# Kernel tuning notes

Measured on AMD Instinct MI355X. Metric: run time of the kernel, lower is better.

## Reference

```python
import jax, jax.numpy as jnp
from jax import lax
import numpy as np

B, N, C = 4, 2000, 80           # images, proposals/img, foreground classes
SCORE_THR = 0.05
IOU_THR = 0.5
MAX_PER_IMG = 100
K_PRE = 2000                     # pre-NMS top-k candidates per image
STDS = np.array([0.1, 0.1, 0.2, 0.2], dtype=np.float32)
MAX_RATIO = float(abs(np.log(16.0 / 1000.0)))  # wh_ratio_clip=16/1000


def setup_inputs() -> dict:
    key = jax.random.key(0)
    k1, k2, k3 = jax.random.split(key, 3)
    class_outs = jax.random.normal(k1, (B, N, C + 1), dtype=jnp.float32)
    regression_outs = jax.random.normal(k2, (B, N, C * 4), dtype=jnp.float32) * 0.5
    # random valid proposal boxes inside 800x1333 images (x1<x2, y1<y2)
    xy = jax.random.uniform(k3, (B, N, 2, 2), dtype=jnp.float32)
    xy = xy * jnp.array([1333.0, 800.0], dtype=jnp.float32)
    lo = jnp.min(xy, axis=2)
    hi = jnp.max(xy, axis=2) + 1.0
    boxes = jnp.concatenate([lo, hi], axis=-1)  # [B,N,4] x1,y1,x2,y2
    images_hw = jnp.tile(jnp.array([[800, 1333]], dtype=jnp.int32), (B, 1))
    return {"class_outs": class_outs, "regression_outs": regression_outs,
            "boxes": boxes, "images_hw": images_hw}


def _decode(props, deltas, h, w):
    # props [N,4], deltas [N,C,4] -> decoded boxes [N,C,4], clipped to image
    d = deltas * jnp.asarray(STDS)
    dx, dy, dw, dh = d[..., 0], d[..., 1], d[..., 2], d[..., 3]
    dw = jnp.clip(dw, -MAX_RATIO, MAX_RATIO)
    dh = jnp.clip(dh, -MAX_RATIO, MAX_RATIO)
    px = (props[:, None, 0] + props[:, None, 2]) * 0.5
    py = (props[:, None, 1] + props[:, None, 3]) * 0.5
    pw = props[:, None, 2] - props[:, None, 0]
    ph = props[:, None, 3] - props[:, None, 1]
    gx = px + pw * dx
    gy = py + ph * dy
    gw = pw * jnp.exp(dw)
    gh = ph * jnp.exp(dh)
    x1 = jnp.clip(gx - gw * 0.5, 0.0, w)
    y1 = jnp.clip(gy - gh * 0.5, 0.0, h)
    x2 = jnp.clip(gx + gw * 0.5, 0.0, w)
    y2 = jnp.clip(gy + gh * 0.5, 0.0, h)
    return jnp.stack([x1, y1, x2, y2], axis=-1)


def _pairwise_iou(b):
    # b [K,4] -> iou [K,K]
    area = (b[:, 2] - b[:, 0]) * (b[:, 3] - b[:, 1])
    lt = jnp.maximum(b[:, None, :2], b[None, :, :2])
    rb = jnp.minimum(b[:, None, 2:], b[None, :, 2:])
    wh = jnp.clip(rb - lt, 0.0)
    inter = wh[..., 0] * wh[..., 1]
    return inter / (area[:, None] + area[None, :] - inter + 1e-6)


def _process_image(cls_out, reg_out, props, hw):
    h = hw[0].astype(jnp.float32)
    w = hw[1].astype(jnp.float32)
    scores = jax.nn.softmax(cls_out, axis=-1)[:, :C]          # drop background col
    bboxes = _decode(props, reg_out.reshape(N, C, 4), h, w)   # [N,C,4]
    flat_scores = scores.reshape(-1)                          # [N*C]
    flat_boxes = bboxes.reshape(-1, 4)
    labels = jnp.tile(jnp.arange(C, dtype=jnp.int32), N)      # class fastest-varying
    cand = jnp.where(flat_scores > SCORE_THR, flat_scores, -1.0)
    top_scores, top_idx = lax.top_k(cand, K_PRE)
    top_boxes = flat_boxes[top_idx]
    top_labels = labels[top_idx]
    valid = top_scores > SCORE_THR
    # class-offset trick: boxes of distinct classes never overlap
    off = top_labels.astype(jnp.float32)[:, None] * (jnp.maximum(h, w) + 1.0)
    iou = _pairwise_iou(top_boxes + off)                      # [K_PRE,K_PRE]
    idxs = jnp.arange(K_PRE)

    def body(i, keep):
        sup = (idxs > i) & (iou[i] > IOU_THR) & keep[i]
        return keep & ~sup

    keep = lax.fori_loop(0, K_PRE, body, valid)
    kept_scores = jnp.where(keep, top_scores, -1.0)
    det_scores, det_i = lax.top_k(kept_scores, MAX_PER_IMG)
    det_valid = det_scores > SCORE_THR
    det_boxes = jnp.where(det_valid[:, None], top_boxes[det_i], 0.0)
    det_labels = jnp.where(det_valid, top_labels[det_i], -1)
    det_scores = jnp.where(det_valid, det_scores, 0.0)
    return det_boxes, det_scores, det_labels


def reference(class_outs, regression_outs, boxes, images_hw):
    det_boxes, det_scores, det_labels = jax.vmap(_process_image)(
        class_outs, regression_outs, boxes, images_hw)
    return det_boxes, det_scores, det_labels
```

## Files before the change

### kernel.cpp

```cpp
#include <hip/hip_runtime.h>


typedef unsigned long long u64;
typedef unsigned int u32;

#define B_ 4
#define N_ 2000
#define C_ 80
#define NCLS 81
#define KPRE 2000
#define MAXDET 100
#define TARGET 192
#define NB 2312
#define NBPAD 2368
#define NG 37
#define HBASE 0xF500
#define KSHIFT 46
#define CAPA 256
#define CAPB 2048
#define CAPIMG 8192
#define KPT 8
#define BPI 125
#define BIGI 0x7fffffff

#define WS_GCUR  0
#define WS_GHIST 64
#define WS_GFLAG 37952
#define WS_GKEYS 38016
#define WS_ZEND  37952

__device__ __forceinline__ u64 pack_key(float score, unsigned fi) {
  return ((u64)__float_as_uint(score) << 32) | (u64)(0xFFFFFFFFu - fi);
}
__device__ __forceinline__ int bucket_of_bits(u32 sb) {
  return min(max((int)(sb >> 14) - HBASE, 0), NB - 1);
}

__device__ __forceinline__ float wred_max(float v) {
  int t;
#define STEPM(ctrl)                                                          \
  t = __builtin_amdgcn_update_dpp(__float_as_int(v), __float_as_int(v),      \
                                  (ctrl), 0xF, 0xF, false);                  \
  v = fmaxf(v, __int_as_float(t));
  STEPM(0x111) STEPM(0x112) STEPM(0x114) STEPM(0x118) STEPM(0x142) STEPM(0x143)
#undef STEPM
  return __int_as_float(__builtin_amdgcn_readlane(__float_as_int(v), 63));
}
__device__ __forceinline__ float wred_sum(float v) {
  int t;
#define STEPS(ctrl)                                                          \
  t = __builtin_amdgcn_update_dpp(0, __float_as_int(v), (ctrl), 0xF, 0xF,    \
                                  false);                                    \
  v = v + __int_as_float(t);
  STEPS(0x111) STEPS(0x112) STEPS(0x114) STEPS(0x118) STEPS(0x142) STEPS(0x143)
#undef STEPS
  return __int_as_float(__builtin_amdgcn_readlane(__float_as_int(v), 63));
}

__device__ __forceinline__ int dpp_min8(int v) {
  int t;
  t = __builtin_amdgcn_update_dpp(BIGI, v, 0x104, 0xF, 0xF, false);
  v = min(v, t);
  t = __builtin_amdgcn_update_dpp(BIGI, v, 0x102, 0xF, 0xF, false);
  v = min(v, t);
  t = __builtin_amdgcn_update_dpp(BIGI, v, 0x101, 0xF, 0xF, false);
  v = min(v, t);
  return v;
}

__device__ __forceinline__ float4 decode_one(
    u64 kk, const float* __restrict__ reg, const float* __restrict__ props,
    int b, float h, float w, float offscale) {
  const float MAXR = 4.135166556742356f;
  unsigned fi = 0xFFFFFFFFu - (u32)kk;
  int n = (int)(fi / (unsigned)C_);
  int c = (int)(fi - (unsigned)n * (unsigned)C_);
  float4 p = ((const float4*)props)[b * N_ + n];
  const float* dl = reg + ((size_t)(b * N_ + n)) * (C_ * 4) + c * 4;
  float dx = dl[0] * 0.1f;
  float dy = dl[1] * 0.1f;
  float dw = fminf(fmaxf(dl[2] * 0.2f, -MAXR), MAXR);
  float dh = fminf(fmaxf(dl[3] * 0.2f, -MAXR), MAXR);
  float px = (p.x + p.z) * 0.5f, py = (p.y + p.w) * 0.5f;
  float pw = p.z - p.x, ph = p.w - p.y;
  float gx = px + pw * dx, gy = py + ph * dy;
  float gw = pw * expf(dw), gh = ph * expf(dh);
  float off = (float)c * offscale;
  return make_float4(fminf(fmaxf(gx - gw * 0.5f, 0.0f), w) + off,
                     fminf(fmaxf(gy - gh * 0.5f, 0.0f), h) + off,
                     fminf(fmaxf(gx + gw * 0.5f, 0.0f), w) + off,
                     fminf(fmaxf(gy + gh * 0.5f, 0.0f), h) + off);
}

__global__ __launch_bounds__(1024) void cand_kernel(
    const float* __restrict__ cls, u64* __restrict__ gkeys,
    u32* __restrict__ gcur, u32* __restrict__ ghist) {
  __shared__ int s_wc[16], s_woff[16];
  __shared__ int s_base;
  const int tid = threadIdx.x;
  const int w = tid >> 6, lane = tid & 63;
  const int blk = blockIdx.x;
  const int b = blk / BPI;
  const int n = (blk % BPI) * 16 + w;
  const float* lg = cls + (size_t)(b * N_ + n) * NCLS;
  float x0 = lg[lane];
  float x1 = (lane < 17) ? lg[64 + lane] : -3.0e38f;
  float mx = wred_max(fmaxf(x0, x1));
  float e0 = expf(x0 - mx);
  float e1 = (lane < 17) ? expf(x1 - mx) : 0.0f;
  float sum = wred_sum(e0 + e1);
  float sc0 = e0 / sum, sc1 = e1 / sum;
  bool p0 = sc0 > 0.05f;
  bool p1 = (lane < 16) && (sc1 > 0.05f);
  u64 m0 = __ballot(p0), m1 = __ballot(p1);
  int c0 = __popcll(m0);
  if (lane == 0) s_wc[w] = c0 + __popcll(m1);
  __syncthreads();
  if (tid == 0) {
    int acc = 0;
#pragma unroll
    for (int i = 0; i < 16; ++i) { s_woff[i] = acc; acc += s_wc[i]; }
    s_base = (acc > 0) ? (int)atomicAdd(&gcur[b], (u32)acc) : 0;
  }
  __syncthreads();
  const int base = s_base + s_woff[w];
  const u64 lt = (1ull << lane) - 1;
  u64* gk = gkeys + (size_t)b * CAPIMG;
  u32* gh = ghist + (size_t)b * NBPAD;
  if (p0) {
    int slot = base + __popcll(m0 & lt);
    if (slot < CAPIMG) gk[slot] = pack_key(sc0, (unsigned)(n * C_ + lane));
    atomicAdd(&gh[bucket_of_bits(__float_as_uint(sc0))], 1u);
  }
  if (p1) {
    int slot = base + c0 + __popcll(m1 & lt);
    if (slot < CAPIMG) gk[slot] = pack_key(sc1, (unsigned)(n * C_ + 64 + lane));
    atomicAdd(&gh[bucket_of_bits(__float_as_uint(sc1))], 1u);
  }
}

__global__ __launch_bounds__(1024) void nmsA_kernel(
    const float* __restrict__ reg, const float* __restrict__ props,
    const int* __restrict__ hw, const u64* __restrict__ gkeys,
    const u32* __restrict__ gcur, const u32* __restrict__ ghist,
    int* __restrict__ gflag, float* __restrict__ out) {
  __shared__ u64 lds8[2156];
  char* bp = (char*)lds8;
  u64* SS = (u64*)bp;
  u64* U = (u64*)(bp + 2048);
  u64* rb = (u64*)(bp + 4128);
  float4* bxA = (float4*)(bp + 12320);
  int* outl = (int*)(bp + 16416);
  int* misc = (int*)(bp + 16928);
  int* s_coarse = (int*)(bp + 16992);

  const int b = blockIdx.x, tid = threadIdx.x;
  const int wv = tid >> 6, lane = tid & 63;

  float h = (float)hw[b * 2 + 0];
  float w = (float)hw[b * 2 + 1];
  float offscale = fmaxf(h, w) + 1.0f;

  if (tid < 16) misc[tid] = 0;
  if (tid >= NG && tid < 64) s_coarse[tid] = 0;

  const u64* keys = gkeys + (size_t)b * CAPIMG;
  const u32 Mraw = gcur[b];
  const int M = min((int)Mraw, CAPIMG);
  if (tid == 0 && Mraw > (u32)CAPIMG) misc[7] = 1;
  u64 kreg[KPT];
#pragma unroll
  for (int r = 0; r < KPT; r++) {
    int idx = tid + (r << 10);
    kreg[r] = (idx < M) ? keys[idx] : 0ULL;
  }
  if (wv >= 12) {
    int g0 = (wv == 12) ? 0 : 10 + (wv - 13) * 9;
    int g1 = (wv == 12) ? 10 : g0 + 9;
    for (int g2 = g0; g2 < g1; g2++) {
      int v = (int)ghist[b * NBPAD + ((g2 << 6) | lane)];
#pragma unroll
      for (int o = 32; o; o >>= 1) v += __shfl_xor(v, o);
      if (lane == 0) s_coarse[g2] = v;
    }
  }
  __syncthreads();

  if (tid < 64) {
    int v = s_coarse[lane];
#pragma unroll
    for (int off = 1; off < 64; off <<= 1) {
      int src = lane + off;
      int o = __shfl(v, src < 64 ? src : 63);
      if (src < 64) v += o;
    }
    int Mtot = __shfl(v, 0);
    u64 pm = __ballot(v >= TARGET);
    int T_A = 0, S_A;
    if (pm) {
      int gs = 63 - __builtin_clzll(pm);
      int beyond = __shfl(v, gs + 1);
      int fv = (int)ghist[b * NBPAD + ((gs << 6) | lane)];
#pragma unroll
      for (int off = 1; off < 64; off <<= 1) {
        int src = lane + off;
        int o = __shfl(fv, src < 64 ? src : 63);
        if (src < 64) fv += o;
      }
      int cum = beyond + fv;
      u64 pm2 = __ballot(cum >= TARGET);
      int tr = 63 - __builtin_clzll(pm2);
      T_A = (gs << 6) + tr;
      S_A = __shfl(cum, tr);
    } else {
      S_A = Mtot;
    }
    if (lane == 0) { misc[0] = T_A; misc[2] = S_A; misc[3] = Mtot; }
  }
  __syncthreads();

  const int T_A = misc[0], S_A = misc[2], Mtot = misc[3];
  bool modeB = (S_A > CAPA) || (misc[7] != 0);
  int K = 0, nkept = 0;

  if (!modeB) {
    {
      const u64 lt = (1ull << lane) - 1;
#pragma unroll
      for (int r = 0; r < KPT; r++) {
        int idx = tid + (r << 10);
        bool pr = (idx < M) &&
                  (bucket_of_bits((u32)(kreg[r] >> 32)) >= T_A);
        u64 mk = __ballot(pr);
        if (mk) {
          int wbase = 0;
          if (lane == 0) wbase = atomicAdd(&misc[4], __popcll(mk));
          wbase = __shfl(wbase, 0);
          if (pr) {
            int pos = wbase + __popcll(mk & lt);
            if (pos < CAPA) U[pos] = kreg[r];
          }
        }
      }
    }
    __syncthreads();
    int S = misc[4];
    if (S > CAPA) S = CAPA;

    if (tid == 0 && (S & 1)) U[S] = 0ULL;
    __syncthreads();
    if (tid < S) {
      u64 k1 = U[tid];
      int r1 = 0;
      const ulonglong2* Uu2 = (const ulonglong2*)U;
      int half = (S + 1) >> 1;
      for (int k = 0; k < half; k++) {
        ulonglong2 kk = Uu2[k];
        r1 += (kk.x > k1) + (kk.y > k1);
      }
      SS[r1] = k1;
    }
    __syncthreads();
    K = S;
    for (int j = tid; j < K; j += 1024)
      bxA[j] = decode_one(SS[j], reg, props, b, h, w, offscale);
    __syncthreads();

    int nwords = (S + 63) >> 6;
    int ntiles = nwords * (nwords + 1) / 2;
    for (int t = wv; t < ntiles; t += 16) {
      int ti = 0, rem = t;
      while (rem >= nwords - ti) { rem -= nwords - ti; ti++; }
      int tj = ti + rem;
      int i = (ti << 6) + lane;
      float4 bi4 = bxA[i];
      float ai = (bi4.z - bi4.x) * (bi4.w - bi4.y);
      u64 bits = 0;
      int jbase = tj << 6;
      int jcount = min(64, S - jbase);
      for (int jj = 0; jj < jcount; jj++) {
        int j = jbase + jj;
        float4 bj = bxA[j];
        float aj = (bj.z - bj.x) * (bj.w - bj.y);
        float iw = fmaxf(fminf(bi4.z, bj.z) - fmaxf(bi4.x, bj.x), 0.0f);
        float ih = fmaxf(fminf(bi4.w, bj.w) - fmaxf(bi4.y, bj.y), 0.0f);
        float inter = iw * ih;
        float iou = inter / (ai + aj - inter + 1e-6f);
        if (j > i && iou > 0.5f) bits |= (1ull << jj);
      }
      if (i < S) rb[i * 4 + tj] = bits;
    }
    __syncthreads();

    if (tid < 64) {
      int nw7 = (S + 63) >> 6;
      u64 alive = 0;
      if (lane < nw7) {
        alive = ~0ull;
        int remb = S & 63;
        if (lane == nw7 - 1 && remb) alive = (1ull << remb) - 1;
      }
      int nk = 0;
      if (S > 0) {
        int i = 0;
        u64 row = (lane < nw7) ? rb[0 * 4 + lane] : 0ull;
        for (;;) {
          if (lane == 0) outl[nk] = i;
          nk++;
          if (nk >= MAXDET) break;
          if (lane == (i >> 6)) alive &= ~(1ull << (i & 63));
          u64 rowSpec = (i + 1 < S && lane < nw7) ? rb[(i + 1) * 4 + lane] : 0ull;
          u64 a2 = alive & ~row;
          alive = a2;
          int cnd = a2 ? ((lane << 6) + (int)__builtin_ctzll(a2)) : BIGI;
          int m8 = dpp_min8(cnd);
          int ni = __builtin_amdgcn_readfirstlane(m8);
          if (ni >= BIGI) break;
          row = (ni == i + 1) ? rowSpec
                              : ((lane < nw7) ? rb[ni * 4 + lane] : 0ull);
          i = ni;
        }
      }
      if (lane == 0) misc[6] = nk;
    }
    __syncthreads();
    nkept = misc[6];
    if (nkept < MAXDET && K < Mtot && K < KPRE) modeB = true;
  }

  if (tid == 0) gflag[b] = modeB ? 1 : 0;
  if (modeB) return;

  float* oBox = out;
  float* oSc = out + B_ * MAXDET * 4;
  float* oLb = out + B_ * MAXDET * 5;
  for (int k2 = tid; k2 < MAXDET; k2 += 1024) {
    float4 bb = make_float4(0.0f, 0.0f, 0.0f, 0.0f);
    float sv = 0.0f, lv = -1.0f;
    if (k2 < nkept) {
      int idx = outl[k2];
      u64 kk = SS[idx];
      sv = __uint_as_float((u32)(kk >> 32));
      unsigned fi = 0xFFFFFFFFu - (u32)kk;
      int c = (int)(fi % (unsigned)C_);
      float off = (float)c * offscale;
      float4 ob = bxA[idx];
      bb = make_float4(ob.x - off, ob.y - off, ob.z - off, ob.w - off);
      lv = (float)c;
    }
    oBox[(b * MAXDET + k2) * 4 + 0] = bb.x;
    oBox[(b * MAXDET + k2) * 4 + 1] = bb.y;
    oBox[(b * MAXDET + k2) * 4 + 2] = bb.z;
    oBox[(b * MAXDET + k2) * 4 + 3] = bb.w;
    oSc[b * MAXDET + k2] = sv;
    oLb[b * MAXDET + k2] = lv;
  }
}

__global__ __launch_bounds__(1024) void nmsB_kernel(
    const float* __restrict__ reg, const float* __restrict__ props,
    const int* __restrict__ hw, const u64* __restrict__ gkeys,
    const u32* __restrict__ gcur, const int* __restrict__ gflag,
    float* __restrict__ out) {
  const int b = blockIdx.x, tid = threadIdx.x;
  if (gflag[b] == 0) return;

  __shared__ u64 lds8[7952];
  char* bp = (char*)lds8;
  u32* hist = (u32*)(bp + 0);
  u64* U2 = (u64*)(bp + 9472);
  u64* SSB = (u64*)(bp + 25856);
  int* outl = (int*)(bp + 42240);
  int* misc = (int*)(bp + 42752);
  const int lane = tid & 63;

  float h = (float)hw[b * 2 + 0];
  float w = (float)hw[b * 2 + 1];
  float offscale = fmaxf(h, w) + 1.0f;

  const u64* keys = gkeys + (size_t)b * CAPIMG;
  const int M = min((int)gcur[b], CAPIMG);

  for (int i = tid; i < NBPAD; i += 1024) hist[i] = 0;
  if (tid < 16) misc[tid] = 0;
  __syncthreads();

  for (int idx = tid; idx < M; idx += 1024) {
    u64 key = keys[idx];
    int bi = min(max((int)(key >> KSHIFT) - HBASE, 0), NB - 1);
    atomicAdd(&hist[bi], 1u);
  }
  __syncthreads();

  if (tid == 0) {
    int acc = 0, tb = 0;
    for (int bi = NB - 1; bi >= 0; bi--) {
      acc += (int)hist[bi];
      if (acc >= KPRE) { tb = bi; break; }
    }
    if (acc > CAPB) tb = min(tb + 1, NB - 1);
    misc[1] = tb;
    misc[4] = 0;
  }
  __syncthreads();
  int T_B = misc[1];

  for (int idx0 = 0; idx0 < M; idx0 += 1024) {
    int idx = idx0 + tid;
    bool pred = false;
    u64 key = 0;
    if (idx < M) {
      key = keys[idx];
      int bi = min(max((int)(key >> KSHIFT) - HBASE, 0), NB - 1);
      pred = (bi >= T_B);
    }
    u64 mk = __ballot(pred);
    if (mk) {
      int wbase = 0;
      if (lane == 0) wbase = atomicAdd(&misc[4], __popcll(mk));
      wbase = __shfl(wbase, 0);
      if (pred) {
        int pos = wbase + __popcll(mk & ((1ull << lane) - 1));
        if (pos < CAPB) U2[pos] = key;
      }
    }
  }
  __syncthreads();
  int S = misc[4];
  if (S > CAPB) S = CAPB;
  {
    int j1 = tid, j2 = tid + 1024;
    u64 k1 = (j1 < S) ? U2[j1] : 0ULL;
    u64 k2 = (j2 < S) ? U2[j2] : 0ULL;
    int r1 = 0, r2 = 0;
    for (int k = 0; k < S; k++) {
      u64 kk = U2[k];
      r1 += (kk > k1);
      r2 += (kk > k2);
    }
    __syncthreads();
    if (j1 < S) SSB[r1] = k1;
    if (j2 < S) SSB[r2] = k2;
  }
  __syncthreads();
  int K = (S < KPRE) ? S : KPRE;
  int j1 = tid, j2 = tid + 1024;
  bool kp1 = (j1 < K), kp2 = (j2 < K);
  float4 bb1 = kp1 ? decode_one(SSB[j1], reg, props, b, h, w, offscale)
                   : make_float4(0, 0, 0, 0);
  float4 bb2 = kp2 ? decode_one(SSB[j2], reg, props, b, h, w, offscale)
                   : make_float4(0, 0, 0, 0);
  int nk = 0;
  if (K > 0) {
    int i = 0;
    for (;;) {
      if (tid == 0) { outl[nk] = i; misc[5] = K; }
      nk++;
      if (nk >= MAXDET) break;
      __syncthreads();
      float4 tb = decode_one(SSB[i], reg, props, b, h, w, offscale);
      float ai = (tb.z - tb.x) * (tb.w - tb.y);
      int ln = K;
      if (kp1 && j1 > i) {
        float aj = (bb1.z - bb1.x) * (bb1.w - bb1.y);
        float iw = fmaxf(fminf(tb.z, bb1.z) - fmaxf(tb.x, bb1.x), 0.0f);
        float ih = fmaxf(fminf(tb.w, bb1.w) - fmaxf(tb.y, bb1.y), 0.0f);
        float inter = iw * ih;
        float iou = inter / (ai + aj - inter + 1e-6f);
        if (iou > 0.5f) kp1 = false;
        else ln = min(ln, j1);
      }
      if (kp2 && j2 > i) {
        float aj = (bb2.z - bb2.x) * (bb2.w - bb2.y);
        float iw = fmaxf(fminf(tb.z, bb2.z) - fmaxf(tb.x, bb2.x), 0.0f);
        float ih = fmaxf(fminf(tb.w, bb2.w) - fmaxf(tb.y, bb2.y), 0.0f);
        float inter = iw * ih;
        float iou = inter / (ai + aj - inter + 1e-6f);
        if (iou > 0.5f) kp2 = false;
        else ln = min(ln, j2);
      }
#pragma unroll
      for (int off = 32; off; off >>= 1) ln = min(ln, __shfl_xor(ln, off));
      if ((tid & 63) == 0 && ln < K) atomicMin(&misc[5], ln);
      __syncthreads();
      int ni = misc[5];
      __syncthreads();
      if (ni >= K) break;
      i = ni;
    }
  }
  if (tid == 0) misc[6] = nk;
  __syncthreads();
  int nkept = misc[6];

  float* oBox = out;
  float* oSc = out + B_ * MAXDET * 4;
  float* oLb = out + B_ * MAXDET * 5;
  for (int k2 = tid; k2 < MAXDET; k2 += 1024) {
    float4 bb = make_float4(0.0f, 0.0f, 0.0f, 0.0f);
    float sv = 0.0f, lv = -1.0f;
    if (k2 < nkept) {
      int idx = outl[k2];
      u64 kk = SSB[idx];
      sv = __uint_as_float((u32)(kk >> 32));
      unsigned fi = 0xFFFFFFFFu - (u32)kk;
      int c = (int)(fi % (unsigned)C_);
      float off = (float)c * offscale;
      float4 ob = decode_one(kk, reg, props, b, h, w, offscale);
      bb = make_float4(ob.x - off, ob.y - off, ob.z - off, ob.w - off);
      lv = (float)c;
    }
    oBox[(b * MAXDET + k2) * 4 + 0] = bb.x;
    oBox[(b * MAXDET + k2) * 4 + 1] = bb.y;
    oBox[(b * MAXDET + k2) * 4 + 2] = bb.z;
    oBox[(b * MAXDET + k2) * 4 + 3] = bb.w;
    oSc[b * MAXDET + k2] = sv;
    oLb[b * MAXDET + k2] = lv;
  }
}

extern "C" void kernel_launch(void* const* d_in, const int* in_sizes, int n_in,
                              void* d_out, int out_size, void* d_ws, size_t ws_size,
                              hipStream_t stream) {
  const float* cls = (const float*)d_in[0];
  const float* reg = (const float*)d_in[1];
  const float* props = (const float*)d_in[2];
  const int* hw = (const int*)d_in[3];
  float* out = (float*)d_out;

  u32* gcur = (u32*)((char*)d_ws + WS_GCUR);
  u32* ghist = (u32*)((char*)d_ws + WS_GHIST);
  int* gflag = (int*)((char*)d_ws + WS_GFLAG);
  u64* gkeys = (u64*)((char*)d_ws + WS_GKEYS);

  hipMemsetAsync(d_ws, 0, WS_ZEND, stream);
  cand_kernel<<<B_ * BPI, 1024, 0, stream>>>(cls, gkeys, gcur, ghist);
  nmsA_kernel<<<B_, 1024, 0, stream>>>(reg, props, hw, gkeys, gcur, ghist,
                                       gflag, out);
  nmsB_kernel<<<B_, 1024, 0, stream>>>(reg, props, hw, gkeys, gcur, gflag, out);
}
```

Measured before the change: 109.5 us.

## Split NMS fast path into mask-build and scan kernels; overlap decode with rank sort

Splits the fast-path NMS into two kernels. The first builds the suppression bitmask and writes sorted keys, boxes and mask rows to workspace. A new 256-thread kernel then runs the serial greedy scan and writes the outputs. Box decoding now runs on unsorted candidates in parallel with the rank sort and is scattered into sorted order afterwards. The histogram is cached in LDS, and key loads no longer wait on the candidate count. This adds a kernel launch and a global round trip for the intermediates, so the gain relies on the shorter per-kernel critical path.

Result: no change. 110.4 us (+0.9%).

```diff
diff --git a/kernel.cpp b/kernel.cpp
--- a/kernel.cpp
+++ b/kernel.cpp
@@ -26,7 +26,11 @@
 #define WS_GCUR  0
 #define WS_GHIST 64
 #define WS_GFLAG 37952
-#define WS_GKEYS 38016
+#define WS_GMETA 37968
+#define WS_GSS   38016
+#define WS_GBX   46208
+#define WS_GRB   62592
+#define WS_GKEYS 95360
 #define WS_ZEND  37952
 
 __device__ __forceinline__ u64 pack_key(float score, unsigned fi) {
@@ -143,16 +147,19 @@
     const float* __restrict__ reg, const float* __restrict__ props,
     const int* __restrict__ hw, const u64* __restrict__ gkeys,
     const u32* __restrict__ gcur, const u32* __restrict__ ghist,
-    int* __restrict__ gflag, float* __restrict__ out) {
-  __shared__ u64 lds8[2156];
+    int* __restrict__ gflag, int* __restrict__ gmeta,
+    u64* __restrict__ gss, float4* __restrict__ gbx, u64* __restrict__ grb) {
+  __shared__ u64 lds8[3914];
   char* bp = (char*)lds8;
-  u64* SS = (u64*)bp;
-  u64* U = (u64*)(bp + 2048);
-  u64* rb = (u64*)(bp + 4128);
-  float4* bxA = (float4*)(bp + 12320);
-  int* outl = (int*)(bp + 16416);
-  int* misc = (int*)(bp + 16928);
-  int* s_coarse = (int*)(bp + 16992);
+  u64* U = (u64*)bp;
+  u64* SS = (u64*)(bp + 2064);
+  u64* rb = (u64*)(bp + 4112);
+  float4* bxU = (float4*)(bp + 12304);
+  float4* bxA = (float4*)(bp + 16400);
+  u32* s_hist = (u32*)(bp + 20496);
+  int* rankA = (int*)(bp + 29968);
+  int* s_coarse = (int*)(bp + 30992);
+  int* misc = (int*)(bp + 31248);
 
   const int b = blockIdx.x, tid = threadIdx.x;
   const int wv = tid >> 6, lane = tid & 63;
@@ -165,20 +172,20 @@
   if (tid >= NG && tid < 64) s_coarse[tid] = 0;
 
   const u64* keys = gkeys + (size_t)b * CAPIMG;
-  const u32 Mraw = gcur[b];
-  const int M = min((int)Mraw, CAPIMG);
-  if (tid == 0 && Mraw > (u32)CAPIMG) misc[7] = 1;
   u64 kreg[KPT];
 #pragma unroll
-  for (int r = 0; r < KPT; r++) {
-    int idx = tid + (r << 10);
-    kreg[r] = (idx < M) ? keys[idx] : 0ULL;
+  for (int r = 0; r < KPT; r++) kreg[r] = keys[tid + (r << 10)];
+  if (tid == 0) {
+    u32 Mraw = gcur[b];
+    misc[5] = min((int)Mraw, CAPIMG);
+    if (Mraw > (u32)CAPIMG) misc[7] = 1;
   }
   if (wv >= 12) {
     int g0 = (wv == 12) ? 0 : 10 + (wv - 13) * 9;
     int g1 = (wv == 12) ? 10 : g0 + 9;
     for (int g2 = g0; g2 < g1; g2++) {
       int v = (int)ghist[b * NBPAD + ((g2 << 6) | lane)];
+      s_hist[(g2 << 6) | lane] = (u32)v;
 #pragma unroll
       for (int o = 32; o; o >>= 1) v += __shfl_xor(v, o);
       if (lane == 0) s_coarse[g2] = v;
@@ -200,7 +207,7 @@
     if (pm) {
       int gs = 63 - __builtin_clzll(pm);
       int beyond = __shfl(v, gs + 1);
-      int fv = (int)ghist[b * NBPAD + ((gs << 6) | lane)];
+      int fv = (int)s_hist[(gs << 6) | lane];
 #pragma unroll
       for (int off = 1; off < 64; off <<= 1) {
         int src = lane + off;
@@ -219,36 +226,37 @@
   }
   __syncthreads();
 
-  const int T_A = misc[0], S_A = misc[2], Mtot = misc[3];
-  bool modeB = (S_A > CAPA) || (misc[7] != 0);
-  int K = 0, nkept = 0;
-
-  if (!modeB) {
-    {
-      const u64 lt = (1ull << lane) - 1;
-#pragma unroll
-      for (int r = 0; r < KPT; r++) {
-        int idx = tid + (r << 10);
-        bool pr = (idx < M) &&
-                  (bucket_of_bits((u32)(kreg[r] >> 32)) >= T_A);
-        u64 mk = __ballot(pr);
-        if (mk) {
-          int wbase = 0;
-          if (lane == 0) wbase = atomicAdd(&misc[4], __popcll(mk));
-          wbase = __shfl(wbase, 0);
-          if (pr) {
-            int pos = wbase + __popcll(mk & lt);
-            if (pos < CAPA) U[pos] = kreg[r];
-          }
+  const int T_A = misc[0], S_A = misc[2], Mtot = misc[3], M = misc[5];
+  if (S_A > CAPA || misc[7] != 0) {
+    if (tid == 0) gflag[b] = 1;
+    return;
+  }
+
+  {
+    const u64 lt = (1ull << lane) - 1;
+#pragma unroll
+    for (int r = 0; r < KPT; r++) {
+      int idx = tid + (r << 10);
+      bool pr = (idx < M) && (bucket_of_bits((u32)(kreg[r] >> 32)) >= T_A);
+      u64 mk = __ballot(pr);
+      if (mk) {
+        int wbase = 0;
+        if (lane == 0) wbase = atomicAdd(&misc[4], __popcll(mk));
+        wbase = __shfl(wbase, 0);
+        if (pr) {
+          int pos = wbase + __popcll(mk & lt);
+          if (pos < CAPA) U[pos] = kreg[r];
         }
       }
     }
-    __syncthreads();
-    int S = misc[4];
-    if (S > CAPA) S = CAPA;
-
-    if (tid == 0 && (S & 1)) U[S] = 0ULL;
-    __syncthreads();
+  }
+  __syncthreads();
+  int S = misc[4];
+  if (S > CAPA) S = CAPA;
+  if (tid == 0 && (S & 1)) U[S] = 0ULL;
+  __syncthreads();
+
+  if (tid < 256) {
     if (tid < S) {
       u64 k1 = U[tid];
       int r1 = 0;
@@ -258,93 +266,139 @@
         ulonglong2 kk = Uu2[k];
         r1 += (kk.x > k1) + (kk.y > k1);
       }
+      rankA[tid] = r1;
       SS[r1] = k1;
     }
-    __syncthreads();
-    K = S;
-    for (int j = tid; j < K; j += 1024)
-      bxA[j] = decode_one(SS[j], reg, props, b, h, w, offscale);
-    __syncthreads();
-
-    int nwords = (S + 63) >> 6;
-    int ntiles = nwords * (nwords + 1) / 2;
-    for (int t = wv; t < ntiles; t += 16) {
-      int ti = 0, rem = t;
-      while (rem >= nwords - ti) { rem -= nwords - ti; ti++; }
-      int tj = ti + rem;
-      int i = (ti << 6) + lane;
-      float4 bi4 = bxA[i];
-      float ai = (bi4.z - bi4.x) * (bi4.w - bi4.y);
-      u64 bits = 0;
-      int jbase = tj << 6;
-      int jcount = min(64, S - jbase);
-      for (int jj = 0; jj < jcount; jj++) {
-        int j = jbase + jj;
-        float4 bj = bxA[j];
-        float aj = (bj.z - bj.x) * (bj.w - bj.y);
-        float iw = fmaxf(fminf(bi4.z, bj.z) - fmaxf(bi4.x, bj.x), 0.0f);
-        float ih = fmaxf(fminf(bi4.w, bj.w) - fmaxf(bi4.y, bj.y), 0.0f);
-        float inter = iw * ih;
-        float iou = inter / (ai + aj - inter + 1e-6f);
-        if (j > i && iou > 0.5f) bits |= (1ull << jj);
+  } else if (tid < 512) {
+    int j = tid - 256;
+    if (j < S) bxU[j] = decode_one(U[j], reg, props, b, h, w, offscale);
+  }
+  __syncthreads();
+  if (tid < S) bxA[rankA[tid]] = bxU[tid];
+  __syncthreads();
+
+  int nwords = (S + 63) >> 6;
+  int ntiles = nwords * (nwords + 1) / 2;
+  for (int t = wv; t < ntiles; t += 16) {
+    int ti = 0, rem = t;
+    while (rem >= nwords - ti) { rem -= nwords - ti; ti++; }
+    int tj = ti + rem;
+    int i = (ti << 6) + lane;
+    float4 bi4 = bxA[i];
+    float ai = (bi4.z - bi4.x) * (bi4.w - bi4.y);
+    u64 bits = 0;
+    int jbase = tj << 6;
+    int jcount = min(64, S - jbase);
+    for (int jj = 0; jj < jcount; jj++) {
+      int j = jbase + jj;
+      float4 bj = bxA[j];
+      float aj = (bj.z - bj.x) * (bj.w - bj.y);
+      float iw = fmaxf(fminf(bi4.z, bj.z) - fmaxf(bi4.x, bj.x), 0.0f);
+      float ih = fmaxf(fminf(bi4.w, bj.w) - fmaxf(bi4.y, bj.y), 0.0f);
+      float inter = iw * ih;
+      float iou = inter / (ai + aj - inter + 1e-6f);
+      if (j > i && iou > 0.5f) bits |= (1ull << jj);
+    }
+    if (i < S) rb[i * 4 + tj] = bits;
+  }
+  __syncthreads();
+
+  if (tid < 256) {
+    if (tid < S) gss[b * CAPA + tid] = SS[tid];
+  } else if (tid < 512) {
+    int j = tid - 256;
+    if (j < S) gbx[b * CAPA + j] = bxA[j];
+  }
+  {
+    int i = tid >> 2, wd = tid & 3;
+    if (i < S) grb[b * CAPA * 4 + i * 4 + wd] = rb[i * 4 + wd];
+  }
+  if (tid == 0) {
+    gmeta[b * 2 + 0] = S;
+    gmeta[b * 2 + 1] = Mtot;
+    gflag[b] = 0;
+  }
+}
+
+__global__ __launch_bounds__(256) void scan_kernel(
+    const int* __restrict__ hw, int* __restrict__ gflag,
+    const int* __restrict__ gmeta, const u64* __restrict__ gss,
+    const float4* __restrict__ gbx, const u64* __restrict__ grb,
+    float* __restrict__ out) {
+  __shared__ u64 lds8[1096];
+  char* bp = (char*)lds8;
+  u64* rb = (u64*)bp;
+  int* outl = (int*)(bp + 8192);
+  int* s_nk = (int*)(bp + 8704);
+
+  const int b = blockIdx.x, tid = threadIdx.x;
+  const int lane = tid & 63;
+  if (gflag[b] != 0) return;
+
+  const int S = gmeta[b * 2 + 0];
+  const int Mtot = gmeta[b * 2 + 1];
+#pragma unroll
+  for (int r = 0; r < 4; r++) {
+    int idx = tid + (r << 8);
+    rb[idx] = grb[b * CAPA * 4 + idx];
+  }
+  float h = (float)hw[b * 2 + 0];
+  float w = (float)hw[b * 2 + 1];
+  float offscale = fmaxf(h, w) + 1.0f;
+  __syncthreads();
+
+  if (tid < 64) {
+    int nw7 = (S + 63) >> 6;
+    u64 alive = 0;
+    if (lane < nw7) {
+      alive = ~0ull;
+      int remb = S & 63;
+      if (lane == nw7 - 1 && remb) alive = (1ull << remb) - 1;
+    }
+    int nk = 0;
+    if (S > 0) {
+      int i = 0;
+      u64 row = (lane < nw7) ? rb[0 * 4 + lane] : 0ull;
+      for (;;) {
+        if (lane == 0) outl[nk] = i;
+        nk++;
+        if (nk >= MAXDET) break;
+        if (lane == (i >> 6)) alive &= ~(1ull << (i & 63));
+        u64 rowSpec = (i + 1 < S && lane < nw7) ? rb[(i + 1) * 4 + lane] : 0ull;
+        u64 a2 = alive & ~row;
+        alive = a2;
+        int cnd = a2 ? ((lane << 6) + (int)__builtin_ctzll(a2)) : BIGI;
+        int m8 = dpp_min8(cnd);
+        int ni = __builtin_amdgcn_readfirstlane(m8);
+        if (ni >= BIGI) break;
+        row = (ni == i + 1) ? rowSpec
+                            : ((lane < nw7) ? rb[ni * 4 + lane] : 0ull);
+        i = ni;
       }
-      if (i < S) rb[i * 4 + tj] = bits;
-    }
-    __syncthreads();
-
-    if (tid < 64) {
-      int nw7 = (S + 63) >> 6;
-      u64 alive = 0;
-      if (lane < nw7) {
-        alive = ~0ull;
-        int remb = S & 63;
-        if (lane == nw7 - 1 && remb) alive = (1ull << remb) - 1;
-      }
-      int nk = 0;
-      if (S > 0) {
-        int i = 0;
-        u64 row = (lane < nw7) ? rb[0 * 4 + lane] : 0ull;
-        for (;;) {
-          if (lane == 0) outl[nk] = i;
-          nk++;
-          if (nk >= MAXDET) break;
-          if (lane == (i >> 6)) alive &= ~(1ull << (i & 63));
-          u64 rowSpec = (i + 1 < S && lane < nw7) ? rb[(i + 1) * 4 + lane] : 0ull;
-          u64 a2 = alive & ~row;
-          alive = a2;
-          int cnd = a2 ? ((lane << 6) + (int)__builtin_ctzll(a2)) : BIGI;
-          int m8 = dpp_min8(cnd);
-          int ni = __builtin_amdgcn_readfirstlane(m8);
-          if (ni >= BIGI) break;
-          row = (ni == i + 1) ? rowSpec
-                              : ((lane < nw7) ? rb[ni * 4 + lane] : 0ull);
-          i = ni;
-        }
-      }
-      if (lane == 0) misc[6] = nk;
-    }
-    __syncthreads();
-    nkept = misc[6];
-    if (nkept < MAXDET && K < Mtot && K < KPRE) modeB = true;
-  }
-
-  if (tid == 0) gflag[b] = modeB ? 1 : 0;
-  if (modeB) return;
+    }
+    if (lane == 0) *s_nk = nk;
+  }
+  __syncthreads();
+  const int nkept = *s_nk;
+  if (nkept < MAXDET && S < Mtot && S < KPRE) {
+    if (tid == 0) gflag[b] = 1;
+    return;
+  }
 
   float* oBox = out;
   float* oSc = out + B_ * MAXDET * 4;
   float* oLb = out + B_ * MAXDET * 5;
-  for (int k2 = tid; k2 < MAXDET; k2 += 1024) {
+  for (int k2 = tid; k2 < MAXDET; k2 += 256) {
     float4 bb = make_float4(0.0f, 0.0f, 0.0f, 0.0f);
     float sv = 0.0f, lv = -1.0f;
     if (k2 < nkept) {
       int idx = outl[k2];
-      u64 kk = SS[idx];
+      u64 kk = gss[b * CAPA + idx];
       sv = __uint_as_float((u32)(kk >> 32));
       unsigned fi = 0xFFFFFFFFu - (u32)kk;
       int c = (int)(fi % (unsigned)C_);
       float off = (float)c * offscale;
-      float4 ob = bxA[idx];
+      float4 ob = gbx[b * CAPA + idx];
       bb = make_float4(ob.x - off, ob.y - off, ob.z - off, ob.w - off);
       lv = (float)c;
     }
@@ -531,11 +585,16 @@
   u32* gcur = (u32*)((char*)d_ws + WS_GCUR);
   u32* ghist = (u32*)((char*)d_ws + WS_GHIST);
   int* gflag = (int*)((char*)d_ws + WS_GFLAG);
+  int* gmeta = (int*)((char*)d_ws + WS_GMETA);
+  u64* gss = (u64*)((char*)d_ws + WS_GSS);
+  float4* gbx = (float4*)((char*)d_ws + WS_GBX);
+  u64* grb = (u64*)((char*)d_ws + WS_GRB);
   u64* gkeys = (u64*)((char*)d_ws + WS_GKEYS);
 
   hipMemsetAsync(d_ws, 0, WS_ZEND, stream);
   cand_kernel<<<B_ * BPI, 1024, 0, stream>>>(cls, gkeys, gcur, ghist);
   nmsA_kernel<<<B_, 1024, 0, stream>>>(reg, props, hw, gkeys, gcur, ghist,
-                                       gflag, out);
+                                       gflag, gmeta, gss, gbx, grb);
+  scan_kernel<<<B_, 256, 0, stream>>>(hw, gflag, gmeta, gss, gbx, grb, out);
   nmsB_kernel<<<B_, 1024, 0, stream>>>(reg, props, hw, gkeys, gcur, gflag, out);
 }
```

## Decode candidate boxes in candidate kernel and stream keys in NMS kernel

Applied to the files above, without the earlier changes.

Box decoding moves from the single-block-per-image NMS kernel into the massively parallel candidate kernel. Each candidate's decoded, class-offset box is written to a new workspace buffer, and the NMS kernel gathers the boxes by slot index after ranking. The NMS kernel also caches the histogram in LDS instead of re-reading global memory, and streams keys with one-ahead prefetch instead of holding eight in registers. This takes the dependent reg/props gathers and exp math off the serial critical path. The cost is extra global writes for every candidate passing the threshold, not just the top few hundred.

Result: no change. 109.6 us (+0.1%).

```diff
diff --git a/kernel.cpp b/kernel.cpp
--- a/kernel.cpp
+++ b/kernel.cpp
@@ -22,11 +22,13 @@
 #define KPT 8
 #define BPI 125
 #define BIGI 0x7fffffff
+#define MAXR 4.135166556742356f
 
 #define WS_GCUR  0
 #define WS_GHIST 64
 #define WS_GFLAG 37952
 #define WS_GKEYS 38016
+#define WS_GBOX  300160
 #define WS_ZEND  37952
 
 __device__ __forceinline__ u64 pack_key(float score, unsigned fi) {
@@ -71,7 +73,6 @@
 __device__ __forceinline__ float4 decode_one(
     u64 kk, const float* __restrict__ reg, const float* __restrict__ props,
     int b, float h, float w, float offscale) {
-  const float MAXR = 4.135166556742356f;
   unsigned fi = 0xFFFFFFFFu - (u32)kk;
   int n = (int)(fi / (unsigned)C_);
   int c = (int)(fi - (unsigned)n * (unsigned)C_);
@@ -93,15 +94,17 @@
 }
 
 __global__ __launch_bounds__(1024) void cand_kernel(
-    const float* __restrict__ cls, u64* __restrict__ gkeys,
+    const float* __restrict__ cls, const float* __restrict__ reg,
+    const float* __restrict__ props, const int* __restrict__ hw,
+    u64* __restrict__ gkeys, float4* __restrict__ gbox,
     u32* __restrict__ gcur, u32* __restrict__ ghist) {
   __shared__ int s_wc[16], s_woff[16];
   __shared__ int s_base;
   const int tid = threadIdx.x;
-  const int w = tid >> 6, lane = tid & 63;
+  const int wvi = tid >> 6, lane = tid & 63;
   const int blk = blockIdx.x;
   const int b = blk / BPI;
-  const int n = (blk % BPI) * 16 + w;
+  const int n = (blk % BPI) * 16 + wvi;
   const float* lg = cls + (size_t)(b * N_ + n) * NCLS;
   float x0 = lg[lane];
   float x1 = (lane < 17) ? lg[64 + lane] : -3.0e38f;
@@ -114,7 +117,7 @@
   bool p1 = (lane < 16) && (sc1 > 0.05f);
   u64 m0 = __ballot(p0), m1 = __ballot(p1);
   int c0 = __popcll(m0);
-  if (lane == 0) s_wc[w] = c0 + __popcll(m1);
+  if (lane == 0) s_wc[wvi] = c0 + __popcll(m1);
   __syncthreads();
   if (tid == 0) {
     int acc = 0;
@@ -123,66 +126,78 @@
     s_base = (acc > 0) ? (int)atomicAdd(&gcur[b], (u32)acc) : 0;
   }
   __syncthreads();
-  const int base = s_base + s_woff[w];
+  const int base = s_base + s_woff[wvi];
   const u64 lt = (1ull << lane) - 1;
   u64* gk = gkeys + (size_t)b * CAPIMG;
+  float4* gbx = gbox + (size_t)b * CAPIMG;
   u32* gh = ghist + (size_t)b * NBPAD;
-  if (p0) {
-    int slot = base + __popcll(m0 & lt);
-    if (slot < CAPIMG) gk[slot] = pack_key(sc0, (unsigned)(n * C_ + lane));
-    atomicAdd(&gh[bucket_of_bits(__float_as_uint(sc0))], 1u);
-  }
-  if (p1) {
-    int slot = base + c0 + __popcll(m1 & lt);
-    if (slot < CAPIMG) gk[slot] = pack_key(sc1, (unsigned)(n * C_ + 64 + lane));
-    atomicAdd(&gh[bucket_of_bits(__float_as_uint(sc1))], 1u);
-  }
-}
-
-__global__ __launch_bounds__(1024) void nmsA_kernel(
-    const float* __restrict__ reg, const float* __restrict__ props,
+  float hh = (float)hw[b * 2 + 0];
+  float ww = (float)hw[b * 2 + 1];
+  float offscale = fmaxf(hh, ww) + 1.0f;
+  float4 p = ((const float4*)props)[b * N_ + n];
+  float px = (p.x + p.z) * 0.5f, py = (p.y + p.w) * 0.5f;
+  float pw = p.z - p.x, ph = p.w - p.y;
+#pragma unroll 1
+  for (int t = 0; t < 2; t++) {
+    bool pp = t ? p1 : p0;
+    if (!pp) continue;
+    float sc = t ? sc1 : sc0;
+    int c = t ? (64 + lane) : lane;
+    int slot = base + (t ? (c0 + __popcll(m1 & lt)) : __popcll(m0 & lt));
+    atomicAdd(&gh[bucket_of_bits(__float_as_uint(sc))], 1u);
+    if (slot < CAPIMG) {
+      gk[slot] = pack_key(sc, (unsigned)(n * C_ + c));
+      const float4 d4 =
+          *(const float4*)(reg + ((size_t)(b * N_ + n)) * (C_ * 4) + c * 4);
+      float dx = d4.x * 0.1f, dy = d4.y * 0.1f;
+      float dw = fminf(fmaxf(d4.z * 0.2f, -MAXR), MAXR);
+      float dh = fminf(fmaxf(d4.w * 0.2f, -MAXR), MAXR);
+      float gx = px + pw * dx, gy = py + ph * dy;
+      float gw = pw * expf(dw), gh2 = ph * expf(dh);
+      float off = (float)c * offscale;
+      gbx[slot] = make_float4(fminf(fmaxf(gx - gw * 0.5f, 0.0f), ww) + off,
+                              fminf(fmaxf(gy - gh2 * 0.5f, 0.0f), hh) + off,
+                              fminf(fmaxf(gx + gw * 0.5f, 0.0f), ww) + off,
+                              fminf(fmaxf(gy + gh2 * 0.5f, 0.0f), hh) + off);
+    }
+  }
+}
+
+__global__ __launch_bounds__(1024) void nms_kernel(
     const int* __restrict__ hw, const u64* __restrict__ gkeys,
-    const u32* __restrict__ gcur, const u32* __restrict__ ghist,
-    int* __restrict__ gflag, float* __restrict__ out) {
-  __shared__ u64 lds8[2156];
+    const float4* __restrict__ gbox, const u32* __restrict__ gcur,
+    const u32* __restrict__ ghist, int* __restrict__ gflag,
+    float* __restrict__ out) {
+  __shared__ u64 lds8[3596];
   char* bp = (char*)lds8;
-  u64* SS = (u64*)bp;
-  u64* U = (u64*)(bp + 2048);
+  u64* U = (u64*)bp;
+  u64* SS = (u64*)(bp + 2080);
   u64* rb = (u64*)(bp + 4128);
   float4* bxA = (float4*)(bp + 12320);
-  int* outl = (int*)(bp + 16416);
-  int* misc = (int*)(bp + 16928);
-  int* s_coarse = (int*)(bp + 16992);
+  u32* s_hist = (u32*)(bp + 16416);
+  u32* Upos = (u32*)(bp + 25888);
+  int* rankA = (int*)(bp + 26912);
+  int* outl = (int*)(bp + 27936);
+  int* s_coarse = (int*)(bp + 28448);
+  int* misc = (int*)(bp + 28704);
 
   const int b = blockIdx.x, tid = threadIdx.x;
   const int wv = tid >> 6, lane = tid & 63;
 
-  float h = (float)hw[b * 2 + 0];
-  float w = (float)hw[b * 2 + 1];
-  float offscale = fmaxf(h, w) + 1.0f;
-
-  if (tid < 16) misc[tid] = 0;
+  if (tid < 16 && tid != 5 && tid != 7) misc[tid] = 0;
   if (tid >= NG && tid < 64) s_coarse[tid] = 0;
-
-  const u64* keys = gkeys + (size_t)b * CAPIMG;
-  const u32 Mraw = gcur[b];
-  const int M = min((int)Mraw, CAPIMG);
-  if (tid == 0 && Mraw > (u32)CAPIMG) misc[7] = 1;
-  u64 kreg[KPT];
+  if (tid == 512) {
+    u32 Mraw = gcur[b];
+    misc[5] = min((int)Mraw, CAPIMG);
+    misc[7] = (Mraw > (u32)CAPIMG) ? 1 : 0;
+  }
+
+  for (int g2 = wv; g2 < NG; g2 += 16) {
+    int v = (int)ghist[b * NBPAD + ((g2 << 6) | lane)];
+    s_hist[(g2 << 6) | lane] = (u32)v;
 #pragma unroll
-  for (int r = 0; r < KPT; r++) {
-    int idx = tid + (r << 10);
-    kreg[r] = (idx < M) ? keys[idx] : 0ULL;
-  }
-  if (wv >= 12) {
-    int g0 = (wv == 12) ? 0 : 10 + (wv - 13) * 9;
-    int g1 = (wv == 12) ? 10 : g0 + 9;
-    for (int g2 = g0; g2 < g1; g2++) {
-      int v = (int)ghist[b * NBPAD + ((g2 << 6) | lane)];
-#pragma unroll
-      for (int o = 32; o; o >>= 1) v += __shfl_xor(v, o);
-      if (lane == 0) s_coarse[g2] = v;
-    }
+    for (int o = 32; o; o >>= 1) v += __shfl_xor(v, o);
+    if (lane == 0) s_coarse[g2] = v;
   }
   __syncthreads();
 
@@ -200,7 +215,7 @@
     if (pm) {
       int gs = 63 - __builtin_clzll(pm);
       int beyond = __shfl(v, gs + 1);
-      int fv = (int)ghist[b * NBPAD + ((gs << 6) | lane)];
+      int fv = (int)s_hist[(gs << 6) | lane];
 #pragma unroll
       for (int off = 1; off < 64; off <<= 1) {
         int src = lane + off;
@@ -219,126 +234,132 @@
   }
   __syncthreads();
 
-  const int T_A = misc[0], S_A = misc[2], Mtot = misc[3];
-  bool modeB = (S_A > CAPA) || (misc[7] != 0);
-  int K = 0, nkept = 0;
-
-  if (!modeB) {
-    {
-      const u64 lt = (1ull << lane) - 1;
-#pragma unroll
-      for (int r = 0; r < KPT; r++) {
-        int idx = tid + (r << 10);
-        bool pr = (idx < M) &&
-                  (bucket_of_bits((u32)(kreg[r] >> 32)) >= T_A);
-        u64 mk = __ballot(pr);
-        if (mk) {
-          int wbase = 0;
-          if (lane == 0) wbase = atomicAdd(&misc[4], __popcll(mk));
-          wbase = __shfl(wbase, 0);
-          if (pr) {
-            int pos = wbase + __popcll(mk & lt);
-            if (pos < CAPA) U[pos] = kreg[r];
-          }
+  const int T_A = misc[0], S_A = misc[2], Mtot = misc[3], M = misc[5];
+  if (S_A > CAPA || misc[7] != 0) {
+    if (tid == 0) gflag[b] = 1;
+    return;
+  }
+
+  {
+    const u64 lt = (1ull << lane) - 1;
+    const u64* keys = gkeys + (size_t)b * CAPIMG;
+    u64 cur = keys[tid];
+#pragma unroll 1
+    for (int r = 0; r < KPT; r++) {
+      u64 nxt = (r + 1 < KPT) ? keys[tid + ((r + 1) << 10)] : 0ULL;
+      int idx = tid + (r << 10);
+      bool pr = (idx < M) && (bucket_of_bits((u32)(cur >> 32)) >= T_A);
+      u64 mk = __ballot(pr);
+      if (mk) {
+        int wbase = 0;
+        if (lane == 0) wbase = atomicAdd(&misc[4], __popcll(mk));
+        wbase = __shfl(wbase, 0);
+        if (pr) {
+          int pos = wbase + __popcll(mk & lt);
+          if (pos < CAPA) { U[pos] = cur; Upos[pos] = (u32)idx; }
         }
       }
-    }
-    __syncthreads();
-    int S = misc[4];
-    if (S > CAPA) S = CAPA;
-
-    if (tid == 0 && (S & 1)) U[S] = 0ULL;
-    __syncthreads();
-    if (tid < S) {
-      u64 k1 = U[tid];
-      int r1 = 0;
-      const ulonglong2* Uu2 = (const ulonglong2*)U;
-      int half = (S + 1) >> 1;
-      for (int k = 0; k < half; k++) {
-        ulonglong2 kk = Uu2[k];
-        r1 += (kk.x > k1) + (kk.y > k1);
+      cur = nxt;
+    }
+  }
+  __syncthreads();
+  int S = misc[4];
+  if (S > CAPA) S = CAPA;
+  if (tid == 0 && (S & 1)) U[S] = 0ULL;
+  __syncthreads();
+
+  if (tid < S) {
+    u64 k1 = U[tid];
+    int r1 = 0;
+    const ulonglong2* Uu2 = (const ulonglong2*)U;
+    int half = (S + 1) >> 1;
+    for (int k = 0; k < half; k++) {
+      ulonglong2 kk = Uu2[k];
+      r1 += (kk.x > k1) + (kk.y > k1);
+    }
+    rankA[tid] = r1;
+  }
+  __syncthreads();
+  if (tid < S) {
+    int r1 = rankA[tid];
+    SS[r1] = U[tid];
+    bxA[r1] = gbox[(size_t)b * CAPIMG + Upos[tid]];
+  }
+  __syncthreads();
+
+  int nwords = (S + 63) >> 6;
+  int ntiles = nwords * (nwords + 1) / 2;
+  for (int t = wv; t < ntiles; t += 16) {
+    int ti = 0, rem = t;
+    while (rem >= nwords - ti) { rem -= nwords - ti; ti++; }
+    int tj = ti + rem;
+    int i = (ti << 6) + lane;
+    float4 bi4 = bxA[i];
+    float ai = (bi4.z - bi4.x) * (bi4.w - bi4.y);
+    u64 bits = 0;
+    int jbase = tj << 6;
+    int jcount = min(64, S - jbase);
+    for (int jj = 0; jj < jcount; jj++) {
+      int j = jbase + jj;
+      float4 bj = bxA[j];
+      float aj = (bj.z - bj.x) * (bj.w - bj.y);
+      float iw = fmaxf(fminf(bi4.z, bj.z) - fmaxf(bi4.x, bj.x), 0.0f);
+      float ih = fmaxf(fminf(bi4.w, bj.w) - fmaxf(bi4.y, bj.y), 0.0f);
+      float inter = iw * ih;
+      float iou = inter / (ai + aj - inter + 1e-6f);
+      if (j > i && iou > 0.5f) bits |= (1ull << jj);
+    }
+    if (i < S) rb[i * 4 + tj] = bits;
+  }
+  __syncthreads();
+
+  if (tid < 64) {
+    u64 alive = 0;
+    if (lane < nwords) {
+      alive = ~0ull;
+      int remb = S & 63;
+      if (lane == nwords - 1 && remb) alive = (1ull << remb) - 1;
+    }
+    int nk = 0;
+    if (S > 0) {
+      int i = 0;
+      u64 row = (lane < nwords) ? rb[0 * 4 + lane] : 0ull;
+      for (;;) {
+        if (lane == 0) outl[nk] = i;
+        nk++;
+        if (nk >= MAXDET) break;
+        if (lane == (i >> 6)) alive &= ~(1ull << (i & 63));
+        u64 rowSpec = (i + 1 < S && lane < nwords) ? rb[(i + 1) * 4 + lane] : 0ull;
+        u64 a2 = alive & ~row;
+        alive = a2;
+        int cnd = a2 ? ((lane << 6) + (int)__builtin_ctzll(a2)) : BIGI;
+        int m8 = dpp_min8(cnd);
+        int ni = __builtin_amdgcn_readfirstlane(m8);
+        if (ni >= BIGI) break;
+        row = (ni == i + 1) ? rowSpec
+                            : ((lane < nwords) ? rb[ni * 4 + lane] : 0ull);
+        i = ni;
       }
-      SS[r1] = k1;
-    }
-    __syncthreads();
-    K = S;
-    for (int j = tid; j < K; j += 1024)
-      bxA[j] = decode_one(SS[j], reg, props, b, h, w, offscale);
-    __syncthreads();
-
-    int nwords = (S + 63) >> 6;
-    int ntiles = nwords * (nwords + 1) / 2;
-    for (int t = wv; t < ntiles; t += 16) {
-      int ti = 0, rem = t;
-      while (rem >= nwords - ti) { rem -= nwords - ti; ti++; }
-      int tj = ti + rem;
-      int i = (ti << 6) + lane;
-      float4 bi4 = bxA[i];
-      float ai = (bi4.z - bi4.x) * (bi4.w - bi4.y);
-      u64 bits = 0;
-      int jbase = tj << 6;
-      int jcount = min(64, S - jbase);
-      for (int jj = 0; jj < jcount; jj++) {
-        int j = jbase + jj;
-        float4 bj = bxA[j];
-        float aj = (bj.z - bj.x) * (bj.w - bj.y);
-        float iw = fmaxf(fminf(bi4.z, bj.z) - fmaxf(bi4.x, bj.x), 0.0f);
-        float ih = fmaxf(fminf(bi4.w, bj.w) - fmaxf(bi4.y, bj.y), 0.0f);
-        float inter = iw * ih;
-        float iou = inter / (ai + aj - inter + 1e-6f);
-        if (j > i && iou > 0.5f) bits |= (1ull << jj);
-      }
-      if (i < S) rb[i * 4 + tj] = bits;
-    }
-    __syncthreads();
-
-    if (tid < 64) {
-      int nw7 = (S + 63) >> 6;
-      u64 alive = 0;
-      if (lane < nw7) {
-        alive = ~0ull;
-        int remb = S & 63;
-        if (lane == nw7 - 1 && remb) alive = (1ull << remb) - 1;
-      }
-      int nk = 0;
-      if (S > 0) {
-        int i = 0;
-        u64 row = (lane < nw7) ? rb[0 * 4 + lane] : 0ull;
-        for (;;) {
-          if (lane == 0) outl[nk] = i;
-          nk++;
-          if (nk >= MAXDET) break;
-          if (lane == (i >> 6)) alive &= ~(1ull << (i & 63));
-          u64 rowSpec = (i + 1 < S && lane < nw7) ? rb[(i + 1) * 4 + lane] : 0ull;
-          u64 a2 = alive & ~row;
-          alive = a2;
-          int cnd = a2 ? ((lane << 6) + (int)__builtin_ctzll(a2)) : BIGI;
-          int m8 = dpp_min8(cnd);
-          int ni = __builtin_amdgcn_readfirstlane(m8);
-          if (ni >= BIGI) break;
-          row = (ni == i + 1) ? rowSpec
-                              : ((lane < nw7) ? rb[ni * 4 + lane] : 0ull);
-          i = ni;
-        }
-      }
-      if (lane == 0) misc[6] = nk;
-    }
-    __syncthreads();
-    nkept = misc[6];
-    if (nkept < MAXDET && K < Mtot && K < KPRE) modeB = true;
-  }
-
+    }
+    if (lane == 0) misc[6] = nk;
+  }
+  __syncthreads();
+  const int nkept = misc[6];
+  bool modeB = (nkept < MAXDET && S < Mtot && S < KPRE);
   if (tid == 0) gflag[b] = modeB ? 1 : 0;
   if (modeB) return;
 
+  float h = (float)hw[b * 2 + 0];
+  float w = (float)hw[b * 2 + 1];
+  float offscale = fmaxf(h, w) + 1.0f;
   float* oBox = out;
   float* oSc = out + B_ * MAXDET * 4;
   float* oLb = out + B_ * MAXDET * 5;
-  for (int k2 = tid; k2 < MAXDET; k2 += 1024) {
+  if (tid < MAXDET) {
     float4 bb = make_float4(0.0f, 0.0f, 0.0f, 0.0f);
     float sv = 0.0f, lv = -1.0f;
-    if (k2 < nkept) {
-      int idx = outl[k2];
+    if (tid < nkept) {
+      int idx = outl[tid];
       u64 kk = SS[idx];
       sv = __uint_as_float((u32)(kk >> 32));
       unsigned fi = 0xFFFFFFFFu - (u32)kk;
@@ -348,12 +369,12 @@
       bb = make_float4(ob.x - off, ob.y - off, ob.z - off, ob.w - off);
       lv = (float)c;
     }
-    oBox[(b * MAXDET + k2) * 4 + 0] = bb.x;
-    oBox[(b * MAXDET + k2) * 4 + 1] = bb.y;
-    oBox[(b * MAXDET + k2) * 4 + 2] = bb.z;
-    oBox[(b * MAXDET + k2) * 4 + 3] = bb.w;
-    oSc[b * MAXDET + k2] = sv;
-    oLb[b * MAXDET + k2] = lv;
+    oBox[(b * MAXDET + tid) * 4 + 0] = bb.x;
+    oBox[(b * MAXDET + tid) * 4 + 1] = bb.y;
+    oBox[(b * MAXDET + tid) * 4 + 2] = bb.z;
+    oBox[(b * MAXDET + tid) * 4 + 3] = bb.w;
+    oSc[b * MAXDET + tid] = sv;
+    oLb[b * MAXDET + tid] = lv;
   }
 }
 
@@ -532,10 +553,11 @@
   u32* ghist = (u32*)((char*)d_ws + WS_GHIST);
   int* gflag = (int*)((char*)d_ws + WS_GFLAG);
   u64* gkeys = (u64*)((char*)d_ws + WS_GKEYS);
+  float4* gbox = (float4*)((char*)d_ws + WS_GBOX);
 
   hipMemsetAsync(d_ws, 0, WS_ZEND, stream);
-  cand_kernel<<<B_ * BPI, 1024, 0, stream>>>(cls, gkeys, gcur, ghist);
-  nmsA_kernel<<<B_, 1024, 0, stream>>>(reg, props, hw, gkeys, gcur, ghist,
-                                       gflag, out);
+  cand_kernel<<<B_ * BPI, 1024, 0, stream>>>(cls, reg, props, hw,
+                                             gkeys, gbox, gcur, ghist);
+  nms_kernel<<<B_, 1024, 0, stream>>>(hw, gkeys, gbox, gcur, ghist, gflag, out);
   nmsB_kernel<<<B_, 1024, 0, stream>>>(reg, props, hw, gkeys, gcur, gflag, out);
 }
```
